# Optimization experiments

Hardware: AMD Instinct MI355X
Metric: run time of the kernel (lower is better)

## Reference

```python
import jax, jax.numpy as jnp
import numpy as np

N_HEAD = 12
NEG_INF = -10000.0


def setup_inputs() -> dict:
    key = jax.random.key(0)
    k1, k2, k3 = jax.random.split(key, 3)
    B, S, D = 8, 1024, 768
    std = 0.01
    return {
        "hidden_states": jax.random.normal(k1, (B, S, D), dtype=jnp.float32),
        "Wqkv": jax.random.normal(k2, (D, 3 * D), dtype=jnp.float32) * std,
        "bqkv": jnp.zeros((3 * D,), dtype=jnp.float32),
        "Wout": jax.random.normal(k3, (D, D), dtype=jnp.float32) * std,
        "bout": jnp.zeros((D,), dtype=jnp.float32),
    }


def reference(hidden_states, Wqkv, bqkv, Wout, bout):
    B, S, D = hidden_states.shape
    H = N_HEAD
    hd = D // H
    # fused QKV projection
    qkv = hidden_states @ Wqkv + bqkv  # [B,S,3D]
    qkv = qkv.reshape(B, S, 3, H, hd)
    q, k, v = qkv[:, :, 0], qkv[:, :, 1], qkv[:, :, 2]  # [B,S,H,hd]
    q = q.transpose(0, 2, 1, 3)  # [B,H,S,hd]
    k = k.transpose(0, 2, 1, 3)
    v = v.transpose(0, 2, 1, 3)
    scale = 1.0 / jnp.sqrt(jnp.asarray(hd, dtype=hidden_states.dtype))
    scores = jnp.einsum("bhqd,bhkd->bhqk", q, k) * scale  # [B,H,S,S]
    causal = jnp.tril(jnp.ones((S, S), dtype=bool))[None, None]
    scores = jnp.where(causal, scores, jnp.asarray(NEG_INF, scores.dtype))
    probs = jax.nn.softmax(scores, axis=-1)
    # dropout is identity in eval/deterministic mode
    attn = jnp.einsum("bhqk,bhkd->bhqd", probs, v)  # [B,H,S,hd]
    attn = attn.transpose(0, 2, 1, 3).reshape(B, S, D)
    return attn @ Wout + bout
```

## Files before the change

### kernel.cpp

```cpp
#include <hip/hip_runtime.h>
#include <hip/hip_bf16.h>

#define B_   8
#define S_   1024
#define D_   768
#define H_   12
#define HD_  64
#define BS_  (B_*S_)
#define N3_  (3*D_)

typedef __attribute__((ext_vector_type(8))) short short8;
typedef __attribute__((ext_vector_type(4))) float f32x4;

__device__ __forceinline__ short8 ld8(const __hip_bfloat16* p) {
    return *reinterpret_cast<const short8*>(p);
}
__device__ __forceinline__ void st8(__hip_bfloat16* p, short8 v) {
    *reinterpret_cast<short8*>(p) = v;
}
__device__ __forceinline__ f32x4 mfma16(short8 a, short8 b, f32x4 c) {
    return __builtin_amdgcn_mfma_f32_16x16x32_bf16(a, b, c, 0, 0, 0);
}
__device__ __forceinline__ void async16(const __hip_bfloat16* g, __hip_bfloat16* l) {
    __builtin_amdgcn_global_load_lds((const __attribute__((address_space(1))) void*)g,
                                     (__attribute__((address_space(3))) void*)l,
                                     16, 0, 0);
}
__device__ __forceinline__ float fast_exp2(float x) {
#if __has_builtin(__builtin_amdgcn_exp2f)
    return __builtin_amdgcn_exp2f(x);
#else
    return __expf(x * 0.69314718056f);
#endif
}

__global__ void cast_f32_bf16(const float* __restrict__ in,
                              __hip_bfloat16* __restrict__ out, int n) {
    int i = (blockIdx.x * blockDim.x + threadIdx.x) * 4;
    if (i + 3 < n) {
        float4 v = *reinterpret_cast<const float4*>(in + i);
        out[i + 0] = __float2bfloat16(v.x);
        out[i + 1] = __float2bfloat16(v.y);
        out[i + 2] = __float2bfloat16(v.z);
        out[i + 3] = __float2bfloat16(v.w);
    }
}

__global__ void transpose_cast(const float* __restrict__ in,
                               __hip_bfloat16* __restrict__ out, int R, int C) {
    __shared__ float tile[32][33];
    int c0 = blockIdx.x * 32, r0 = blockIdx.y * 32;
    for (int i = threadIdx.y; i < 32; i += 8) {
        tile[i][threadIdx.x] = in[(size_t)(r0 + i) * C + c0 + threadIdx.x];
    }
    __syncthreads();
    for (int i = threadIdx.y; i < 32; i += 8) {
        out[(size_t)(c0 + i) * R + r0 + threadIdx.x] =
            __float2bfloat16(tile[threadIdx.x][i]);
    }
}

__global__ __launch_bounds__(256)
void gemm_qkv(const __hip_bfloat16* __restrict__ A,
              const __hip_bfloat16* __restrict__ Bt,
              const float* __restrict__ bqkv,
              __hip_bfloat16* __restrict__ Qb,
              __hip_bfloat16* __restrict__ Kb,
              __hip_bfloat16* __restrict__ Vtb) {
    __shared__ __align__(16) char smem[128 * 132 * 2];
    __hip_bfloat16* Ct = (__hip_bfloat16*)smem;

    int tid = threadIdx.x, wave = tid >> 6, lane = tid & 63;
    int ln = lane & 15, quad = lane >> 4;
    int mb = blockIdx.y * 128, nb = blockIdx.x * 128;
    int wm = (wave >> 1) * 64, wn = (wave & 1) * 64;

    f32x4 acc[4][4];
#pragma unroll
    for (int i = 0; i < 4; ++i)
#pragma unroll
        for (int j = 0; j < 4; ++j) acc[i][j] = (f32x4){0.f, 0.f, 0.f, 0.f};

    auto stage = [&](int k, int buf) {
        __hip_bfloat16* Asb = (__hip_bfloat16*)(smem + buf * 16384);
        __hip_bfloat16* Bsb = Asb + 128 * 32;
#pragma unroll
        for (int it = 0; it < 2; ++it) {
            int c = it * 256 + tid;
            int row = c >> 2, cc = c & 3;
            int csw = cc ^ ((row >> 1) & 3);
            async16(A + (size_t)(mb + row) * D_ + k + csw * 8,
                    Asb + it * 2048 + wave * 512);
            async16(Bt + (size_t)(nb + row) * D_ + k + csw * 8,
                    Bsb + it * 2048 + wave * 512);
        }
    };

    stage(0, 0);
    int cur = 0;
    for (int k = 0; k < D_; k += 32) {
        __syncthreads();
        if (k + 32 < D_) stage(k + 32, cur ^ 1);

        __hip_bfloat16* As = (__hip_bfloat16*)(smem + cur * 16384);
        __hip_bfloat16* Bs = As + 128 * 32;
        short8 a[4], b[4];
#pragma unroll
        for (int i = 0; i < 4; ++i) {
            int row = wm + i * 16 + ln;
            a[i] = ld8(As + row * 32 + ((quad ^ ((row >> 1) & 3)) << 3));
        }
#pragma unroll
        for (int j = 0; j < 4; ++j) {
            int row = wn + j * 16 + ln;
            b[j] = ld8(Bs + row * 32 + ((quad ^ ((row >> 1) & 3)) << 3));
        }
#pragma unroll
        for (int i = 0; i < 4; ++i)
#pragma unroll
            for (int j = 0; j < 4; ++j)
                acc[i][j] = mfma16(a[i], b[j], acc[i][j]);
        cur ^= 1;
    }
    __syncthreads();

    int which = blockIdx.x / 6;
    int nbr = nb - which * D_;
    float qscale = (which == 0) ? (0.125f * 1.44269504089f) : 1.f;

#pragma unroll
    for (int j = 0; j < 4; ++j) {
        int col = wn + j * 16 + ln;
        float bias = bqkv[nb + col];
#pragma unroll
        for (int i = 0; i < 4; ++i)
#pragma unroll
            for (int r = 0; r < 4; ++r) {
                int row = wm + i * 16 + quad * 4 + r;
                __hip_bfloat16 v = __float2bfloat16((acc[i][j][r] + bias) * qscale);
                if (which != 2) Ct[row * 132 + col] = v;
                else            Ct[col * 132 + row] = v;
            }
    }
    __syncthreads();

    int bb = mb >> 10, sb = mb & 1023;
    if (which != 2) {
        __hip_bfloat16* dst = (which == 0) ? Qb : Kb;
#pragma unroll
        for (int it = 0; it < 8; ++it) {
            int cc = it * 256 + tid;
            int row = cc >> 4, c8 = cc & 15;
            short8 v = ld8(Ct + row * 132 + c8 * 8);
            int gcol = nbr + c8 * 8;
            int h = gcol >> 6, d = gcol & 63;
            int s = sb + row;
            st8(dst + (((size_t)(bb * H_ + h)) * S_ + s) * HD_ + d, v);
        }
    } else {
#pragma unroll
        for (int it = 0; it < 8; ++it) {
            int cc = it * 256 + tid;
            int drow = cc >> 4, s8 = cc & 15;
            short8 v = ld8(Ct + drow * 132 + s8 * 8);
            int gd = nbr + drow;
            int h = gd >> 6, d = gd & 63;
            st8(Vtb + ((size_t)(bb * H_ + h) * HD_ + d) * S_ + sb + s8 * 8, v);
        }
    }
}

__global__ __launch_bounds__(256, 3)
void attn_flash3(const __hip_bfloat16* __restrict__ Q,
                 const __hip_bfloat16* __restrict__ K,
                 const __hip_bfloat16* __restrict__ Vt,
                 __hip_bfloat16* __restrict__ attnbf) {
    __shared__ __hip_bfloat16 Kbuf[2][64 * 64];
    __shared__ __hip_bfloat16 Vbuf[2][64 * 64];
    __shared__ __hip_bfloat16 Pbuf[4][32 * 72];

    int bh = blockIdx.y;
    int ip = blockIdx.x;
    int tid = threadIdx.x;
    int wave = tid >> 6, lane = tid & 63;
    int ln = lane & 15, quad = lane >> 4;
    int strip = (wave < 2) ? ip : (15 - ip);
    int qrow0 = strip * 64 + (wave & 1) * 32;

    const __hip_bfloat16* Qbh = Q + (size_t)bh * S_ * HD_;
    const __hip_bfloat16* Kbh = K + (size_t)bh * S_ * HD_;
    const __hip_bfloat16* Vbh = Vt + (size_t)bh * HD_ * S_;

    short8 aq[2][2];
#pragma unroll
    for (int rt = 0; rt < 2; ++rt)
#pragma unroll
        for (int ks = 0; ks < 2; ++ks)
            aq[rt][ks] = ld8(Qbh + (size_t)(qrow0 + rt * 16 + ln) * HD_ +
                             ks * 32 + quad * 8);

    f32x4 o[2][4];
    float l_run[2][4];
#pragma unroll
    for (int rt = 0; rt < 2; ++rt)
#pragma unroll
        for (int n = 0; n < 4; ++n) {
            o[rt][n] = (f32x4){0.f, 0.f, 0.f, 0.f};
            l_run[rt][n] = 0.f;
        }

    int last_kt = 15 - ip;

    auto stage = [&](int kt, int buf) {
        const __hip_bfloat16* gK = Kbh + (size_t)kt * 64 * HD_;
#pragma unroll
        for (int it = 0; it < 2; ++it) {
            int p = it * 256 + tid;
            int row = p >> 3;
            int csw = (p & 7) ^ (row & 7);
            async16(gK + row * HD_ + csw * 8,
                    &Kbuf[buf][it * 2048 + wave * 512]);
            async16(Vbh + (size_t)row * S_ + kt * 64 + csw * 8,
                    &Vbuf[buf][it * 2048 + wave * 512]);
        }
    };

    stage(0, 0);
    __syncthreads();
    int cur = 0;

    for (int kt = 0; kt <= last_kt; ++kt) {
        int kbase = kt * 64;
        if (kt < last_kt) stage(kt + 1, cur ^ 1);

        if (kbase <= qrow0 + 31) {
            const __hip_bfloat16* Kc = Kbuf[cur];
            const __hip_bfloat16* Vc = Vbuf[cur];

            f32x4 s[2][4];
#pragma unroll
            for (int rt = 0; rt < 2; ++rt)
#pragma unroll
                for (int j = 0; j < 4; ++j) s[rt][j] = (f32x4){0.f, 0.f, 0.f, 0.f};
#pragma unroll
            for (int j = 0; j < 4; ++j) {
                int row = j * 16 + ln;
#pragma unroll
                for (int ks = 0; ks < 2; ++ks) {
                    short8 bk = ld8(&Kc[row * 64 +
                                        (((ks * 4 + quad) ^ (row & 7)) << 3)]);
#pragma unroll
                    for (int rt = 0; rt < 2; ++rt)
                        s[rt][j] = mfma16(aq[rt][ks], bk, s[rt][j]);
                }
            }

            if (kbase + 63 > qrow0) {
#pragma unroll
                for (int rt = 0; rt < 2; ++rt)
#pragma unroll
                    for (int j = 0; j < 4; ++j) {
                        int key = kbase + j * 16 + ln;
#pragma unroll
                        for (int r = 0; r < 4; ++r) {
                            int q = qrow0 + rt * 16 + quad * 4 + r;
                            if (key > q) s[rt][j][r] = -INFINITY;
                        }
                    }
            }

#pragma unroll
            for (int rt = 0; rt < 2; ++rt)
#pragma unroll
                for (int j = 0; j < 4; ++j)
#pragma unroll
                    for (int r = 0; r < 4; ++r)
                        s[rt][j][r] = fast_exp2(s[rt][j][r]);
#pragma unroll
            for (int rt = 0; rt < 2; ++rt)
#pragma unroll
                for (int r = 0; r < 4; ++r)
                    l_run[rt][r] += (s[rt][0][r] + s[rt][1][r]) +
                                    (s[rt][2][r] + s[rt][3][r]);

#pragma unroll
            for (int rt = 0; rt < 2; ++rt)
#pragma unroll
                for (int j = 0; j < 4; ++j)
#pragma unroll
                    for (int r = 0; r < 4; ++r)
                        Pbuf[wave][(rt * 16 + quad * 4 + r) * 72 + j * 16 + ln] =
                            __float2bfloat16(s[rt][j][r]);
            asm volatile("s_waitcnt lgkmcnt(0)" ::: "memory");

            short8 ap[2][2];
#pragma unroll
            for (int rt = 0; rt < 2; ++rt)
#pragma unroll
                for (int ks = 0; ks < 2; ++ks)
                    ap[rt][ks] = ld8(&Pbuf[wave][(rt * 16 + ln) * 72 +
                                                 ks * 32 + quad * 8]);

#pragma unroll
            for (int n = 0; n < 4; ++n) {
                int row = n * 16 + ln;
#pragma unroll
                for (int ks = 0; ks < 2; ++ks) {
                    short8 bv = ld8(&Vc[row * 64 +
                                        (((ks * 4 + quad) ^ (row & 7)) << 3)]);
#pragma unroll
                    for (int rt = 0; rt < 2; ++rt)
                        o[rt][n] = mfma16(ap[rt][ks], bv, o[rt][n]);
                }
            }
        }

        __syncthreads();
        cur ^= 1;
    }

    int bb = bh / H_, h = bh - bb * H_;
#pragma unroll
    for (int rt = 0; rt < 2; ++rt)
#pragma unroll
        for (int r = 0; r < 4; ++r) {
            float l = l_run[rt][r];
            l += __shfl_xor(l, 1);
            l += __shfl_xor(l, 2);
            l += __shfl_xor(l, 4);
            l += __shfl_xor(l, 8);
            float inv = 1.f / l;
            int row = qrow0 + rt * 16 + quad * 4 + r;
#pragma unroll
            for (int n = 0; n < 4; ++n) {
                int col = h * 64 + n * 16 + ln;
                attnbf[((size_t)bb * S_ + row) * D_ + col] =
                    __float2bfloat16(o[rt][n][r] * inv);
            }
        }
}

__global__ __launch_bounds__(256)
void gemm_out(const __hip_bfloat16* __restrict__ A,
              const __hip_bfloat16* __restrict__ Bt,
              const float* __restrict__ bias,
              float* __restrict__ Cout) {
    __shared__ __align__(16) char smem[2 * 16384];

    int tid = threadIdx.x, wave = tid >> 6, lane = tid & 63;
    int ln = lane & 15, quad = lane >> 4;
    int mb = blockIdx.y * 128, nb = blockIdx.x * 128;
    int wm = (wave >> 1) * 64, wn = (wave & 1) * 64;

    f32x4 acc[4][4];
#pragma unroll
    for (int i = 0; i < 4; ++i)
#pragma unroll
        for (int j = 0; j < 4; ++j) acc[i][j] = (f32x4){0.f, 0.f, 0.f, 0.f};

    auto stage = [&](int k, int buf) {
        __hip_bfloat16* Asb = (__hip_bfloat16*)(smem + buf * 16384);
        __hip_bfloat16* Bsb = Asb + 128 * 32;
#pragma unroll
        for (int it = 0; it < 2; ++it) {
            int c = it * 256 + tid;
            int row = c >> 2, cc = c & 3;
            int csw = cc ^ ((row >> 1) & 3);
            async16(A + (size_t)(mb + row) * D_ + k + csw * 8,
                    Asb + it * 2048 + wave * 512);
            async16(Bt + (size_t)(nb + row) * D_ + k + csw * 8,
                    Bsb + it * 2048 + wave * 512);
        }
    };

    stage(0, 0);
    int cur = 0;
    for (int k = 0; k < D_; k += 32) {
        __syncthreads();
        if (k + 32 < D_) stage(k + 32, cur ^ 1);

        __hip_bfloat16* As = (__hip_bfloat16*)(smem + cur * 16384);
        __hip_bfloat16* Bs = As + 128 * 32;
        short8 a[4], b[4];
#pragma unroll
        for (int i = 0; i < 4; ++i) {
            int row = wm + i * 16 + ln;
            a[i] = ld8(As + row * 32 + ((quad ^ ((row >> 1) & 3)) << 3));
        }
#pragma unroll
        for (int j = 0; j < 4; ++j) {
            int row = wn + j * 16 + ln;
            b[j] = ld8(Bs + row * 32 + ((quad ^ ((row >> 1) & 3)) << 3));
        }
#pragma unroll
        for (int i = 0; i < 4; ++i)
#pragma unroll
            for (int j = 0; j < 4; ++j)
                acc[i][j] = mfma16(a[i], b[j], acc[i][j]);
        cur ^= 1;
    }

#pragma unroll
    for (int j = 0; j < 4; ++j) {
        int col = nb + wn + j * 16 + ln;
        float bv = bias[col];
#pragma unroll
        for (int i = 0; i < 4; ++i)
#pragma unroll
            for (int r = 0; r < 4; ++r) {
                int row = mb + wm + i * 16 + quad * 4 + r;
                Cout[(size_t)row * D_ + col] = acc[i][j][r] + bv;
            }
    }
}

extern "C" void kernel_launch(void* const* d_in, const int* in_sizes, int n_in,
                              void* d_out, int out_size, void* d_ws, size_t ws_size,
                              hipStream_t stream) {
    const float* X    = (const float*)d_in[0];
    const float* Wqkv = (const float*)d_in[1];
    const float* bqkv = (const float*)d_in[2];
    const float* Wout = (const float*)d_in[3];
    const float* bout = (const float*)d_in[4];
    float* out = (float*)d_out;

    constexpr size_t SZ_XBF   = (size_t)BS_ * D_ * 2;
    constexpr size_t SZ_WQKVT = (size_t)N3_ * D_ * 2;
    constexpr size_t SZ_WOUTT = (size_t)D_ * D_ * 2;
    constexpr size_t SZ_QKV   = (size_t)B_ * H_ * S_ * HD_ * 2;

    char* w = (char*)d_ws;
    __hip_bfloat16* Xbf    = (__hip_bfloat16*)(w);
    __hip_bfloat16* WqkvT  = (__hip_bfloat16*)(w + SZ_XBF);
    __hip_bfloat16* WoutT  = (__hip_bfloat16*)(w + SZ_XBF + SZ_WQKVT);
    __hip_bfloat16* Qb     = (__hip_bfloat16*)(w + SZ_XBF + SZ_WQKVT + SZ_WOUTT);
    __hip_bfloat16* Kb     = (__hip_bfloat16*)(w + SZ_XBF + SZ_WQKVT + SZ_WOUTT + SZ_QKV);
    __hip_bfloat16* Vtb    = (__hip_bfloat16*)(w + SZ_XBF + SZ_WQKVT + SZ_WOUTT + 2*SZ_QKV);
    __hip_bfloat16* attnbf = (__hip_bfloat16*)(w + SZ_XBF + SZ_WQKVT + SZ_WOUTT + 3*SZ_QKV);
    (void)ws_size; (void)in_sizes; (void)n_in; (void)out_size;

    int nX = BS_ * D_;
    cast_f32_bf16<<<nX / (256 * 4), 256, 0, stream>>>(X, Xbf, nX);
    transpose_cast<<<dim3(N3_ / 32, D_ / 32), dim3(32, 8), 0, stream>>>(Wqkv, WqkvT, D_, N3_);
    transpose_cast<<<dim3(D_ / 32, D_ / 32), dim3(32, 8), 0, stream>>>(Wout, WoutT, D_, D_);

    gemm_qkv<<<dim3(N3_ / 128, BS_ / 128), 256, 0, stream>>>(Xbf, WqkvT, bqkv, Qb, Kb, Vtb);

    attn_flash3<<<dim3(8, B_ * H_), 256, 0, stream>>>(Qb, Kb, Vtb, attnbf);

    gemm_out<<<dim3(D_ / 128, BS_ / 128), 256, 0, stream>>>(attnbf, WoutT, bout, out);
}
```

Baseline: 192.7 us.

## Triple-buffer GEMM K-loop with partial vmcnt waits instead of full syncthreads

Both the QKV and output projection GEMMs move from double to triple buffering in LDS, prefetching two K-steps ahead. Each iteration waits only until the oldest stage's global-to-LDS loads have landed (vmcnt(4)) and then issues a raw s_barrier, rather than a full __syncthreads that drains every outstanding load. This is meant to hide global load latency behind the MFMA work. It raises LDS use to 48KB per block, which may reduce occupancy, and it relies on the hand-written waitcnt matching the number of loads in flight.

```diff
diff --git a/kernel.cpp b/kernel.cpp
--- a/kernel.cpp
+++ b/kernel.cpp
@@ -67,7 +67,7 @@
               __hip_bfloat16* __restrict__ Qb,
               __hip_bfloat16* __restrict__ Kb,
               __hip_bfloat16* __restrict__ Vtb) {
-    __shared__ __align__(16) char smem[128 * 132 * 2];
+    __shared__ __align__(16) char smem[49152];
     __hip_bfloat16* Ct = (__hip_bfloat16*)smem;
 
     int tid = threadIdx.x, wave = tid >> 6, lane = tid & 63;
@@ -81,8 +81,8 @@
 #pragma unroll
         for (int j = 0; j < 4; ++j) acc[i][j] = (f32x4){0.f, 0.f, 0.f, 0.f};
 
-    auto stage = [&](int k, int buf) {
-        __hip_bfloat16* Asb = (__hip_bfloat16*)(smem + buf * 16384);
+    auto stage = [&](int k, int bufoff) {
+        __hip_bfloat16* Asb = (__hip_bfloat16*)(smem + bufoff);
         __hip_bfloat16* Bsb = Asb + 128 * 32;
 #pragma unroll
         for (int it = 0; it < 2; ++it) {
@@ -96,13 +96,8 @@
         }
     };
 
-    stage(0, 0);
-    int cur = 0;
-    for (int k = 0; k < D_; k += 32) {
-        __syncthreads();
-        if (k + 32 < D_) stage(k + 32, cur ^ 1);
-
-        __hip_bfloat16* As = (__hip_bfloat16*)(smem + cur * 16384);
+    auto compute = [&](int bufoff) {
+        __hip_bfloat16* As = (__hip_bfloat16*)(smem + bufoff);
         __hip_bfloat16* Bs = As + 128 * 32;
         short8 a[4], b[4];
 #pragma unroll
@@ -120,8 +115,24 @@
 #pragma unroll
             for (int j = 0; j < 4; ++j)
                 acc[i][j] = mfma16(a[i], b[j], acc[i][j]);
-        cur ^= 1;
-    }
+    };
+
+    stage(0, 0);
+    stage(32, 16384);
+    int cb = 0;
+    for (int k = 0; k < D_ - 32; k += 32) {
+        asm volatile("s_waitcnt vmcnt(4)" ::: "memory");
+        asm volatile("s_barrier" ::: "memory");
+        if (k + 64 < D_) {
+            int sb = cb + 32768; if (sb >= 49152) sb -= 49152;
+            stage(k + 64, sb);
+        }
+        compute(cb);
+        cb += 16384; if (cb >= 49152) cb = 0;
+    }
+    asm volatile("s_waitcnt vmcnt(0)" ::: "memory");
+    asm volatile("s_barrier" ::: "memory");
+    compute(cb);
     __syncthreads();
 
     int which = blockIdx.x / 6;
@@ -345,7 +356,7 @@
               const __hip_bfloat16* __restrict__ Bt,
               const float* __restrict__ bias,
               float* __restrict__ Cout) {
-    __shared__ __align__(16) char smem[2 * 16384];
+    __shared__ __align__(16) char smem[49152];
 
     int tid = threadIdx.x, wave = tid >> 6, lane = tid & 63;
     int ln = lane & 15, quad = lane >> 4;
@@ -358,8 +369,8 @@
 #pragma unroll
         for (int j = 0; j < 4; ++j) acc[i][j] = (f32x4){0.f, 0.f, 0.f, 0.f};
 
-    auto stage = [&](int k, int buf) {
-        __hip_bfloat16* Asb = (__hip_bfloat16*)(smem + buf * 16384);
+    auto stage = [&](int k, int bufoff) {
+        __hip_bfloat16* Asb = (__hip_bfloat16*)(smem + bufoff);
         __hip_bfloat16* Bsb = Asb + 128 * 32;
 #pragma unroll
         for (int it = 0; it < 2; ++it) {
@@ -373,13 +384,8 @@
         }
     };
 
-    stage(0, 0);
-    int cur = 0;
-    for (int k = 0; k < D_; k += 32) {
-        __syncthreads();
-        if (k + 32 < D_) stage(k + 32, cur ^ 1);
-
-        __hip_bfloat16* As = (__hip_bfloat16*)(smem + cur * 16384);
+    auto compute = [&](int bufoff) {
+        __hip_bfloat16* As = (__hip_bfloat16*)(smem + bufoff);
         __hip_bfloat16* Bs = As + 128 * 32;
         short8 a[4], b[4];
 #pragma unroll
@@ -397,8 +403,24 @@
 #pragma unroll
             for (int j = 0; j < 4; ++j)
                 acc[i][j] = mfma16(a[i], b[j], acc[i][j]);
-        cur ^= 1;
-    }
+    };
+
+    stage(0, 0);
+    stage(32, 16384);
+    int cb = 0;
+    for (int k = 0; k < D_ - 32; k += 32) {
+        asm volatile("s_waitcnt vmcnt(4)" ::: "memory");
+        asm volatile("s_barrier" ::: "memory");
+        if (k + 64 < D_) {
+            int sb = cb + 32768; if (sb >= 49152) sb -= 49152;
+            stage(k + 64, sb);
+        }
+        compute(cb);
+        cb += 16384; if (cb >= 49152) cb = 0;
+    }
+    asm volatile("s_waitcnt vmcnt(0)" ::: "memory");
+    asm volatile("s_barrier" ::: "memory");
+    compute(cb);
 
 #pragma unroll
     for (int j = 0; j < 4; ++j) {
```

Result: no change. 192.4 us (-0.1%).

## Merge prep kernels and load GEMM B operand directly into registers

Applied to the files above, without the earlier changes.

Three preprocessing launches (X cast and two weight transpose-casts) are merged into one launch, with the block index selecting the task, to cut launch overhead. In both GEMMs the B (weight) tile now goes straight from global memory into registers with a one-step register prefetch, and only A is staged through LDS. This halves LDS use and LDS traffic per block and replaces __syncthreads with explicit vmcnt waits plus s_barrier. The trade-off is uncoalesced 16-byte global loads for B that each wave issues on its own, and the hand-written waitcnt counts must match the real number of outstanding loads to stay correct.

```diff
diff --git a/kernel.cpp b/kernel.cpp
--- a/kernel.cpp
+++ b/kernel.cpp
@@ -34,30 +34,39 @@
 #endif
 }
 
-__global__ void cast_f32_bf16(const float* __restrict__ in,
-                              __hip_bfloat16* __restrict__ out, int n) {
-    int i = (blockIdx.x * blockDim.x + threadIdx.x) * 4;
-    if (i + 3 < n) {
-        float4 v = *reinterpret_cast<const float4*>(in + i);
-        out[i + 0] = __float2bfloat16(v.x);
-        out[i + 1] = __float2bfloat16(v.y);
-        out[i + 2] = __float2bfloat16(v.z);
-        out[i + 3] = __float2bfloat16(v.w);
-    }
-}
-
-__global__ void transpose_cast(const float* __restrict__ in,
-                               __hip_bfloat16* __restrict__ out, int R, int C) {
+__global__ __launch_bounds__(256)
+void prep_inputs(const float* __restrict__ X,
+                 const float* __restrict__ Wqkv,
+                 const float* __restrict__ Wout,
+                 __hip_bfloat16* __restrict__ Xbf,
+                 __hip_bfloat16* __restrict__ WqkvT,
+                 __hip_bfloat16* __restrict__ WoutT) {
     __shared__ float tile[32][33];
-    int c0 = blockIdx.x * 32, r0 = blockIdx.y * 32;
-    for (int i = threadIdx.y; i < 32; i += 8) {
-        tile[i][threadIdx.x] = in[(size_t)(r0 + i) * C + c0 + threadIdx.x];
-    }
+    int bid = blockIdx.x, tid = threadIdx.x;
+    if (bid < 6144) {
+        int i = (bid * 256 + tid) * 4;
+        float4 v = *reinterpret_cast<const float4*>(X + i);
+        Xbf[i + 0] = __float2bfloat16(v.x);
+        Xbf[i + 1] = __float2bfloat16(v.y);
+        Xbf[i + 2] = __float2bfloat16(v.z);
+        Xbf[i + 3] = __float2bfloat16(v.w);
+        return;
+    }
+    const float* in; __hip_bfloat16* out; int R, C, bx, by;
+    if (bid < 6144 + 1728) {
+        int t = bid - 6144; in = Wqkv; out = WqkvT; R = D_; C = N3_;
+        bx = t % 72; by = t / 72;
+    } else {
+        int t = bid - 6144 - 1728; in = Wout; out = WoutT; R = D_; C = D_;
+        bx = t % 24; by = t / 24;
+    }
+    int tx = tid & 31, ty = tid >> 5;
+    int c0 = bx * 32, r0 = by * 32;
+    for (int i = ty; i < 32; i += 8)
+        tile[i][tx] = in[(size_t)(r0 + i) * C + c0 + tx];
     __syncthreads();
-    for (int i = threadIdx.y; i < 32; i += 8) {
-        out[(size_t)(c0 + i) * R + r0 + threadIdx.x] =
-            __float2bfloat16(tile[threadIdx.x][i]);
-    }
+    for (int i = ty; i < 32; i += 8)
+        out[(size_t)(c0 + i) * R + r0 + tx] = __float2bfloat16(tile[tx][i]);
 }
 
 __global__ __launch_bounds__(256)
@@ -81,9 +90,8 @@
 #pragma unroll
         for (int j = 0; j < 4; ++j) acc[i][j] = (f32x4){0.f, 0.f, 0.f, 0.f};
 
-    auto stage = [&](int k, int buf) {
-        __hip_bfloat16* Asb = (__hip_bfloat16*)(smem + buf * 16384);
-        __hip_bfloat16* Bsb = Asb + 128 * 32;
+    auto stageA = [&](int k, int buf) {
+        __hip_bfloat16* Asb = (__hip_bfloat16*)(smem + buf * 8192);
 #pragma unroll
         for (int it = 0; it < 2; ++it) {
             int c = it * 256 + tid;
@@ -91,35 +99,45 @@
             int csw = cc ^ ((row >> 1) & 3);
             async16(A + (size_t)(mb + row) * D_ + k + csw * 8,
                     Asb + it * 2048 + wave * 512);
-            async16(Bt + (size_t)(nb + row) * D_ + k + csw * 8,
-                    Bsb + it * 2048 + wave * 512);
         }
     };
-
-    stage(0, 0);
+    auto loadB = [&](int k, short8* bq) {
+#pragma unroll
+        for (int j = 0; j < 4; ++j)
+            bq[j] = ld8(Bt + (size_t)(nb + wn + j * 16 + ln) * D_ + k + quad * 8);
+    };
+
+    short8 bq[4], bn[4];
+    loadB(0, bq);
+    stageA(0, 0);
     int cur = 0;
     for (int k = 0; k < D_; k += 32) {
-        __syncthreads();
-        if (k + 32 < D_) stage(k + 32, cur ^ 1);
-
-        __hip_bfloat16* As = (__hip_bfloat16*)(smem + cur * 16384);
-        __hip_bfloat16* Bs = As + 128 * 32;
-        short8 a[4], b[4];
+        bool notlast = (k + 32 < D_);
+        if (notlast) {
+            loadB(k + 32, bn);
+            asm volatile("s_waitcnt vmcnt(4)" ::: "memory");
+        } else {
+            asm volatile("s_waitcnt vmcnt(0)" ::: "memory");
+        }
+        asm volatile("s_barrier" ::: "memory");
+        if (notlast) stageA(k + 32, cur ^ 1);
+
+        __hip_bfloat16* As = (__hip_bfloat16*)(smem + cur * 8192);
+        short8 a[4];
 #pragma unroll
         for (int i = 0; i < 4; ++i) {
             int row = wm + i * 16 + ln;
             a[i] = ld8(As + row * 32 + ((quad ^ ((row >> 1) & 3)) << 3));
         }
 #pragma unroll
-        for (int j = 0; j < 4; ++j) {
-            int row = wn + j * 16 + ln;
-            b[j] = ld8(Bs + row * 32 + ((quad ^ ((row >> 1) & 3)) << 3));
-        }
-#pragma unroll
         for (int i = 0; i < 4; ++i)
 #pragma unroll
             for (int j = 0; j < 4; ++j)
-                acc[i][j] = mfma16(a[i], b[j], acc[i][j]);
+                acc[i][j] = mfma16(a[i], bq[j], acc[i][j]);
+        if (notlast) {
+#pragma unroll
+            for (int j = 0; j < 4; ++j) bq[j] = bn[j];
+        }
         cur ^= 1;
     }
     __syncthreads();
@@ -345,7 +363,7 @@
               const __hip_bfloat16* __restrict__ Bt,
               const float* __restrict__ bias,
               float* __restrict__ Cout) {
-    __shared__ __align__(16) char smem[2 * 16384];
+    __shared__ __align__(16) char smem[2 * 8192];
 
     int tid = threadIdx.x, wave = tid >> 6, lane = tid & 63;
     int ln = lane & 15, quad = lane >> 4;
@@ -358,9 +376,8 @@
 #pragma unroll
         for (int j = 0; j < 4; ++j) acc[i][j] = (f32x4){0.f, 0.f, 0.f, 0.f};
 
-    auto stage = [&](int k, int buf) {
-        __hip_bfloat16* Asb = (__hip_bfloat16*)(smem + buf * 16384);
-        __hip_bfloat16* Bsb = Asb + 128 * 32;
+    auto stageA = [&](int k, int buf) {
+        __hip_bfloat16* Asb = (__hip_bfloat16*)(smem + buf * 8192);
 #pragma unroll
         for (int it = 0; it < 2; ++it) {
             int c = it * 256 + tid;
@@ -368,35 +385,45 @@
             int csw = cc ^ ((row >> 1) & 3);
             async16(A + (size_t)(mb + row) * D_ + k + csw * 8,
                     Asb + it * 2048 + wave * 512);
-            async16(Bt + (size_t)(nb + row) * D_ + k + csw * 8,
-                    Bsb + it * 2048 + wave * 512);
         }
     };
-
-    stage(0, 0);
+    auto loadB = [&](int k, short8* bq) {
+#pragma unroll
+        for (int j = 0; j < 4; ++j)
+            bq[j] = ld8(Bt + (size_t)(nb + wn + j * 16 + ln) * D_ + k + quad * 8);
+    };
+
+    short8 bq[4], bn[4];
+    loadB(0, bq);
+    stageA(0, 0);
     int cur = 0;
     for (int k = 0; k < D_; k += 32) {
-        __syncthreads();
-        if (k + 32 < D_) stage(k + 32, cur ^ 1);
-
-        __hip_bfloat16* As = (__hip_bfloat16*)(smem + cur * 16384);
-        __hip_bfloat16* Bs = As + 128 * 32;
-        short8 a[4], b[4];
+        bool notlast = (k + 32 < D_);
+        if (notlast) {
+            loadB(k + 32, bn);
+            asm volatile("s_waitcnt vmcnt(4)" ::: "memory");
+        } else {
+            asm volatile("s_waitcnt vmcnt(0)" ::: "memory");
+        }
+        asm volatile("s_barrier" ::: "memory");
+        if (notlast) stageA(k + 32, cur ^ 1);
+
+        __hip_bfloat16* As = (__hip_bfloat16*)(smem + cur * 8192);
+        short8 a[4];
 #pragma unroll
         for (int i = 0; i < 4; ++i) {
             int row = wm + i * 16 + ln;
             a[i] = ld8(As + row * 32 + ((quad ^ ((row >> 1) & 3)) << 3));
         }
 #pragma unroll
-        for (int j = 0; j < 4; ++j) {
-            int row = wn + j * 16 + ln;
-            b[j] = ld8(Bs + row * 32 + ((quad ^ ((row >> 1) & 3)) << 3));
-        }
-#pragma unroll
         for (int i = 0; i < 4; ++i)
 #pragma unroll
             for (int j = 0; j < 4; ++j)
-                acc[i][j] = mfma16(a[i], b[j], acc[i][j]);
+                acc[i][j] = mfma16(a[i], bq[j], acc[i][j]);
+        if (notlast) {
+#pragma unroll
+            for (int j = 0; j < 4; ++j) bq[j] = bn[j];
+        }
         cur ^= 1;
     }
 
@@ -439,10 +466,8 @@
     __hip_bfloat16* attnbf = (__hip_bfloat16*)(w + SZ_XBF + SZ_WQKVT + SZ_WOUTT + 3*SZ_QKV);
     (void)ws_size; (void)in_sizes; (void)n_in; (void)out_size;
 
-    int nX = BS_ * D_;
-    cast_f32_bf16<<<nX / (256 * 4), 256, 0, stream>>>(X, Xbf, nX);
-    transpose_cast<<<dim3(N3_ / 32, D_ / 32), dim3(32, 8), 0, stream>>>(Wqkv, WqkvT, D_, N3_);
-    transpose_cast<<<dim3(D_ / 32, D_ / 32), dim3(32, 8), 0, stream>>>(Wout, WoutT, D_, D_);
+    prep_inputs<<<6144 + 1728 + 576, 256, 0, stream>>>(X, Wqkv, Wout,
+                                                       Xbf, WqkvT, WoutT);
 
     gemm_qkv<<<dim3(N3_ / 128, BS_ / 128), 256, 0, stream>>>(Xbf, WqkvT, bqkv, Qb, Kb, Vtb);
 
```

Result: slower. 253.9 us (+31.8%).
